# Optimization experiments

Hardware: AMD Instinct MI355X
Metric: run time of the kernel (lower is better)

The kernel has to match this reference:

```python
import jax, jax.numpy as jnp
import numpy as np

NUM_CLASSES = 80
L_BOX, L_OBJ, L_CLS = 5.0, 1.0, 1.0


def setup_inputs() -> dict:
    key = jax.random.key(0)
    k0, k1, k2, k3, k4 = jax.random.split(key, 5)
    B, N = 32, 50
    C = 5 + NUM_CLASSES
    pred0 = jax.random.normal(k0, (B, C, 64, 64), dtype=jnp.float32)
    pred1 = jax.random.normal(k1, (B, C, 32, 32), dtype=jnp.float32)
    pred2 = jax.random.normal(k2, (B, C, 16, 16), dtype=jnp.float32)
    # normalized cxcywh in (0,1)
    boxes = jax.random.uniform(k3, (B, N, 4), dtype=jnp.float32, minval=0.01, maxval=0.99)
    labels = jax.random.randint(k4, (B, N), 0, NUM_CLASSES, dtype=jnp.int32)
    return {"pred0": pred0, "pred1": pred1, "pred2": pred2, "boxes": boxes, "labels": labels}


def _bce_with_logits_mean(x, t):
    # numerically stable BCEWithLogits, mean reduction
    return jnp.mean(jnp.maximum(x, 0.0) - x * t + jnp.log1p(jnp.exp(-jnp.abs(x))))


def _build_targets(boxes, labels, b, h, w):
    # boxes: [B,N,4] normalized cxcywh; labels: [B,N]
    B, N, _ = boxes.shape
    bi = jnp.repeat(jnp.arange(B), N)            # [B*N]
    bf = boxes.reshape(-1, 4)                    # [B*N,4]
    lf = labels.reshape(-1)                      # [B*N]
    gx = bf[:, 0] * w
    gy = bf[:, 1] * h
    gi = jnp.minimum(gx.astype(jnp.int32), w - 1)  # int() truncation; gx >= 0
    gj = jnp.minimum(gy.astype(jnp.int32), h - 1)
    obj_t = jnp.zeros((b, 1, h, w), jnp.float32).at[bi, 0, gj, gi].set(1.0)
    vals = jnp.stack([gx - gi, gy - gj, bf[:, 2], bf[:, 3]], axis=1)  # [B*N,4]
    ch4 = jnp.arange(4)
    box_t = jnp.zeros((b, 4, h, w), jnp.float32).at[
        bi[:, None], ch4[None, :], gj[:, None], gi[:, None]].set(vals)
    cls_t = jnp.zeros((b, NUM_CLASSES, h, w), jnp.float32).at[bi, lf, gj, gi].set(1.0)
    return box_t, obj_t, cls_t


def _scale_loss(pred, boxes, labels):
    b, _, h, w = pred.shape
    box_t, obj_t, cls_t = _build_targets(boxes, labels, b, h, w)
    pb = jnp.clip(pred[:, :4], -10.0, 10.0)
    po = jnp.clip(pred[:, 4:5], -10.0, 10.0)
    pc = jnp.clip(pred[:, 5:], -10.0, 10.0)
    box_loss = jnp.mean((pb - box_t) ** 2)
    obj_loss = _bce_with_logits_mean(po, obj_t)
    cls_loss = _bce_with_logits_mean(pc, cls_t)
    # torch code zeroes non-finite losses; clamped logits keep these finite,
    # mirrored with jnp.where for faithfulness
    box_loss = jnp.where(jnp.isfinite(box_loss), box_loss, 0.0)
    obj_loss = jnp.where(jnp.isfinite(obj_loss), obj_loss, 0.0)
    cls_loss = jnp.where(jnp.isfinite(cls_loss), cls_loss, 0.0)
    return L_BOX * box_loss + L_OBJ * obj_loss + L_CLS * cls_loss


def reference(pred0, pred1, pred2, boxes, labels):
    total = (_scale_loss(pred0, boxes, labels)
             + _scale_loss(pred1, boxes, labels)
             + _scale_loss(pred2, boxes, labels))
    return jnp.clip(total / 3.0, 0.0, 1000000.0)
```

## Files before the change

### kernel.cpp

```cpp
#include <hip/hip_runtime.h>
#include <math.h>

#define NCLS 80
#define BB   32
#define NBOX 50
#define CC   85

#define GRID1 2048
#define BLK1  256

__device__ __forceinline__ float clip10(float x) {
    return fminf(fmaxf(x, -10.f), 10.f);
}

__device__ __forceinline__ float bce0(float x) {
    return fmaxf(x, 0.f) + __logf(1.f + __expf(-fabsf(x)));
}

__global__ __launch_bounds__(BLK1) void base_kernel(
    const float* __restrict__ p0, const float* __restrict__ p1,
    const float* __restrict__ p2,
    const float* __restrict__ boxes, const int* __restrict__ labels,
    double* __restrict__ partial)
{
    const int tid = blockIdx.x * BLK1 + threadIdx.x;
    const int nth = GRID1 * BLK1;
    const float* ps[3] = {p0, p1, p2};
    const int hw4s[3]  = {64*64/4, 32*32/4, 16*16/4};

    float part[9];
    #pragma unroll
    for (int s = 0; s < 3; ++s) {
        const float4* p = (const float4*)ps[s];
        const int hw4 = hw4s[s];
        const int n4  = BB * CC * hw4;
        float bx = 0.f, ob = 0.f, cl = 0.f;
        for (int i = tid; i < n4; i += nth) {
            float4 v = p[i];
            int c = (i / hw4) % CC;
            float a0 = clip10(v.x), a1 = clip10(v.y);
            float a2 = clip10(v.z), a3 = clip10(v.w);
            if (c < 4) {
                bx += a0*a0 + a1*a1 + a2*a2 + a3*a3;
            } else if (c == 4) {
                ob += bce0(a0) + bce0(a1) + bce0(a2) + bce0(a3);
            } else {
                cl += bce0(a0) + bce0(a1) + bce0(a2) + bce0(a3);
            }
        }
        part[3*s+0] = bx; part[3*s+1] = ob; part[3*s+2] = cl;
    }

    __shared__ int   s_cell[NBOX];
    __shared__ int   s_lab[NBOX];
    __shared__ float s_vx[NBOX], s_vy[NBOX], s_vw[NBOX], s_vh[NBOX];

    const bool doCorr = (blockIdx.x < 3 * BB);
    const int  cs = blockIdx.x / BB;
    const int  cb = blockIdx.x % BB;
    const int  Ws[3] = {64, 32, 16};

    if (doCorr && threadIdx.x < 64) {
        const int n = threadIdx.x;
        const int W = Ws[cs];
        if (n < NBOX) {
            const float* bp = boxes + ((size_t)cb * NBOX + n) * 4;
            float gx = bp[0] * (float)W;
            float gy = bp[1] * (float)W;
            int gi = min((int)gx, W - 1);
            int gj = min((int)gy, W - 1);
            s_cell[n] = gj * W + gi;
            s_lab[n]  = labels[cb * NBOX + n];
            s_vx[n] = gx - (float)gi;
            s_vy[n] = gy - (float)gj;
            s_vw[n] = bp[2];
            s_vh[n] = bp[3];
        }
    }
    __syncthreads();
    if (doCorr && threadIdx.x < 64) {
        const int n = threadIdx.x;
        const int W = Ws[cs], hw = W * W;
        const float* pred = ps[cs];
        float cbx = 0.f, cob = 0.f, ccl = 0.f;
        if (n < NBOX) {
            const int cell = s_cell[n], lab = s_lab[n];
            bool lastCell = true, lastCls = true;
            for (int m = n + 1; m < NBOX; ++m) {
                if (s_cell[m] == cell) {
                    lastCell = false;
                    if (s_lab[m] == lab) lastCls = false;
                }
            }
            const float* pb_base = pred + (size_t)(cb * CC) * hw + cell;
            if (lastCell) {
                float vals[4] = {s_vx[n], s_vy[n], s_vw[n], s_vh[n]};
                #pragma unroll
                for (int c = 0; c < 4; ++c) {
                    float pb = clip10(pb_base[c * hw]);
                    float d  = pb - vals[c];
                    cbx += d * d - pb * pb;
                }
                float po = clip10(pb_base[4 * hw]);
                cob -= po;
            }
            if (lastCls) {
                float pc = clip10(pb_base[(5 + lab) * hw]);
                ccl -= pc;
            }
        }
        #pragma unroll
        for (int off = 32; off > 0; off >>= 1) {
            cbx += __shfl_down(cbx, off);
            cob += __shfl_down(cob, off);
            ccl += __shfl_down(ccl, off);
        }
        if (n == 0) {
            part[3*cs+0] += cbx;
            part[3*cs+1] += cob;
            part[3*cs+2] += ccl;
        }
    }

    #pragma unroll
    for (int k = 0; k < 9; ++k) {
        float v = part[k];
        #pragma unroll
        for (int off = 32; off > 0; off >>= 1) v += __shfl_down(v, off);
        part[k] = v;
    }
    __shared__ float sred[BLK1/64][9];
    const int wave = threadIdx.x >> 6;
    const int lane = threadIdx.x & 63;
    if (lane == 0) {
        #pragma unroll
        for (int k = 0; k < 9; ++k) sred[wave][k] = part[k];
    }
    __syncthreads();
    if (threadIdx.x == 0) {
        double* o = partial + (size_t)blockIdx.x * 9;
        #pragma unroll
        for (int k = 0; k < 9; ++k)
            o[k] = (double)(sred[0][k] + sred[1][k] + sred[2][k] + sred[3][k]);
    }
}

__global__ __launch_bounds__(256) void final_kernel(
    const double* __restrict__ partial, float* __restrict__ out, int nb)
{
    double loc[9];
    #pragma unroll
    for (int k = 0; k < 9; ++k) loc[k] = 0.0;
    for (int i = threadIdx.x; i < nb; i += 256) {
        const double* row = partial + (size_t)i * 9;
        #pragma unroll
        for (int k = 0; k < 9; ++k) loc[k] += row[k];
    }
    #pragma unroll
    for (int k = 0; k < 9; ++k) {
        double v = loc[k];
        #pragma unroll
        for (int off = 32; off > 0; off >>= 1) v += __shfl_down(v, off);
        loc[k] = v;
    }
    __shared__ double sred[4][9];
    const int wave = threadIdx.x >> 6;
    const int lane = threadIdx.x & 63;
    if (lane == 0) {
        #pragma unroll
        for (int k = 0; k < 9; ++k) sred[wave][k] = loc[k];
    }
    __syncthreads();
    if (threadIdx.x == 0) {
        const double hws[3] = {4096.0, 1024.0, 256.0};
        double total = 0.0;
        #pragma unroll
        for (int s = 0; s < 3; ++s) {
            double hw  = hws[s];
            double tb = sred[0][3*s+0] + sred[1][3*s+0] + sred[2][3*s+0] + sred[3][3*s+0];
            double to = sred[0][3*s+1] + sred[1][3*s+1] + sred[2][3*s+1] + sred[3][3*s+1];
            double tc = sred[0][3*s+2] + sred[1][3*s+2] + sred[2][3*s+2] + sred[3][3*s+2];
            double box = tb / (32.0 * 4.0 * hw);
            double ob  = to / (32.0 * hw);
            double cl  = tc / (32.0 * 80.0 * hw);
            total += 5.0 * box + ob + cl;
        }
        total /= 3.0;
        total = fmin(fmax(total, 0.0), 1000000.0);
        out[0] = (float)total;
    }
}

extern "C" void kernel_launch(void* const* d_in, const int* in_sizes, int n_in,
                              void* d_out, int out_size, void* d_ws, size_t ws_size,
                              hipStream_t stream)
{
    const float* p0     = (const float*)d_in[0];
    const float* p1     = (const float*)d_in[1];
    const float* p2     = (const float*)d_in[2];
    const float* boxes  = (const float*)d_in[3];
    const int*   labels = (const int*)d_in[4];
    float* out = (float*)d_out;

    double* partial = (double*)d_ws;

    base_kernel<<<GRID1, BLK1, 0, stream>>>(p0, p1, p2, boxes, labels, partial);
    final_kernel<<<1, 256, 0, stream>>>(partial, out, GRID1);
}
```

Before: 105.7 us.

## Fuse final reduction into main kernel via cooperative grid sync

Merges the separate final reduction kernel into the main streaming kernel: all blocks write partials, a cooperative grid-wide sync follows, then block 0 reduces and writes the loss. The grid is halved to 1024 blocks with a launch-bounds occupancy hint so every block can be co-resident, which cooperative launch requires. This removes one kernel launch and its gap, but adds grid-sync overhead and halves the number of blocks streaming the input.

Result: slower. 255.8 us (+142.1%).

```diff
diff --git a/kernel.cpp b/kernel.cpp
--- a/kernel.cpp
+++ b/kernel.cpp
@@ -1,13 +1,17 @@
 #include <hip/hip_runtime.h>
+#include <hip/hip_cooperative_groups.h>
 #include <math.h>
+
+namespace cg = cooperative_groups;
 
 #define NCLS 80
 #define BB   32
 #define NBOX 50
 #define CC   85
 
-#define GRID1 2048
+#define GRID1 1024
 #define BLK1  256
+#define NTH   (GRID1 * BLK1)
 
 __device__ __forceinline__ float clip10(float x) {
     return fminf(fmaxf(x, -10.f), 10.f);
@@ -17,14 +21,13 @@
     return fmaxf(x, 0.f) + __logf(1.f + __expf(-fabsf(x)));
 }
 
-__global__ __launch_bounds__(BLK1) void base_kernel(
+__global__ __launch_bounds__(BLK1, 4) void fused_kernel(
     const float* __restrict__ p0, const float* __restrict__ p1,
     const float* __restrict__ p2,
     const float* __restrict__ boxes, const int* __restrict__ labels,
-    double* __restrict__ partial)
+    double* __restrict__ partial, float* __restrict__ out)
 {
     const int tid = blockIdx.x * BLK1 + threadIdx.x;
-    const int nth = GRID1 * BLK1;
     const float* ps[3] = {p0, p1, p2};
     const int hw4s[3]  = {64*64/4, 32*32/4, 16*16/4};
 
@@ -35,7 +38,7 @@
         const int hw4 = hw4s[s];
         const int n4  = BB * CC * hw4;
         float bx = 0.f, ob = 0.f, cl = 0.f;
-        for (int i = tid; i < n4; i += nth) {
+        for (int i = tid; i < n4; i += NTH) {
             float4 v = p[i];
             int c = (i / hw4) % CC;
             float a0 = clip10(v.x), a1 = clip10(v.y);
@@ -143,51 +146,50 @@
         for (int k = 0; k < 9; ++k)
             o[k] = (double)(sred[0][k] + sred[1][k] + sred[2][k] + sred[3][k]);
     }
-}
-
-__global__ __launch_bounds__(256) void final_kernel(
-    const double* __restrict__ partial, float* __restrict__ out, int nb)
-{
-    double loc[9];
-    #pragma unroll
-    for (int k = 0; k < 9; ++k) loc[k] = 0.0;
-    for (int i = threadIdx.x; i < nb; i += 256) {
-        const double* row = partial + (size_t)i * 9;
-        #pragma unroll
-        for (int k = 0; k < 9; ++k) loc[k] += row[k];
-    }
-    #pragma unroll
-    for (int k = 0; k < 9; ++k) {
-        double v = loc[k];
-        #pragma unroll
-        for (int off = 32; off > 0; off >>= 1) v += __shfl_down(v, off);
-        loc[k] = v;
-    }
-    __shared__ double sred[4][9];
-    const int wave = threadIdx.x >> 6;
-    const int lane = threadIdx.x & 63;
-    if (lane == 0) {
-        #pragma unroll
-        for (int k = 0; k < 9; ++k) sred[wave][k] = loc[k];
-    }
-    __syncthreads();
-    if (threadIdx.x == 0) {
-        const double hws[3] = {4096.0, 1024.0, 256.0};
-        double total = 0.0;
-        #pragma unroll
-        for (int s = 0; s < 3; ++s) {
-            double hw  = hws[s];
-            double tb = sred[0][3*s+0] + sred[1][3*s+0] + sred[2][3*s+0] + sred[3][3*s+0];
-            double to = sred[0][3*s+1] + sred[1][3*s+1] + sred[2][3*s+1] + sred[3][3*s+1];
-            double tc = sred[0][3*s+2] + sred[1][3*s+2] + sred[2][3*s+2] + sred[3][3*s+2];
-            double box = tb / (32.0 * 4.0 * hw);
-            double ob  = to / (32.0 * hw);
-            double cl  = tc / (32.0 * 80.0 * hw);
-            total += 5.0 * box + ob + cl;
-        }
-        total /= 3.0;
-        total = fmin(fmax(total, 0.0), 1000000.0);
-        out[0] = (float)total;
+
+    __threadfence();
+    cg::this_grid().sync();
+
+    if (blockIdx.x == 0) {
+        double loc[9];
+        #pragma unroll
+        for (int k = 0; k < 9; ++k) loc[k] = 0.0;
+        for (int i = threadIdx.x; i < GRID1; i += BLK1) {
+            const double* row = partial + (size_t)i * 9;
+            #pragma unroll
+            for (int k = 0; k < 9; ++k) loc[k] += row[k];
+        }
+        #pragma unroll
+        for (int k = 0; k < 9; ++k) {
+            double v = loc[k];
+            #pragma unroll
+            for (int off = 32; off > 0; off >>= 1) v += __shfl_down(v, off);
+            loc[k] = v;
+        }
+        __shared__ double dred[BLK1/64][9];
+        if (lane == 0) {
+            #pragma unroll
+            for (int k = 0; k < 9; ++k) dred[wave][k] = loc[k];
+        }
+        __syncthreads();
+        if (threadIdx.x == 0) {
+            const double hws[3] = {4096.0, 1024.0, 256.0};
+            double total = 0.0;
+            #pragma unroll
+            for (int s = 0; s < 3; ++s) {
+                double hw = hws[s];
+                double tb = dred[0][3*s+0] + dred[1][3*s+0] + dred[2][3*s+0] + dred[3][3*s+0];
+                double to = dred[0][3*s+1] + dred[1][3*s+1] + dred[2][3*s+1] + dred[3][3*s+1];
+                double tc = dred[0][3*s+2] + dred[1][3*s+2] + dred[2][3*s+2] + dred[3][3*s+2];
+                double box = tb / (32.0 * 4.0 * hw);
+                double ob  = to / (32.0 * hw);
+                double cl  = tc / (32.0 * 80.0 * hw);
+                total += 5.0 * box + ob + cl;
+            }
+            total /= 3.0;
+            total = fmin(fmax(total, 0.0), 1000000.0);
+            out[0] = (float)total;
+        }
     }
 }
 
@@ -204,6 +206,9 @@
 
     double* partial = (double*)d_ws;
 
-    base_kernel<<<GRID1, BLK1, 0, stream>>>(p0, p1, p2, boxes, labels, partial);
-    final_kernel<<<1, 256, 0, stream>>>(partial, out, GRID1);
-}
+    void* args[] = {(void*)&p0, (void*)&p1, (void*)&p2,
+                    (void*)&boxes, (void*)&labels,
+                    (void*)&partial, (void*)&out};
+    hipLaunchCooperativeKernel((const void*)fused_kernel,
+                               dim3(GRID1), dim3(BLK1), args, 0, stream);
+}
```
